# Performance work log

Measured on AMD Instinct MI355X. Metric: run time of the kernel, lower is better.

## Reference

```python
import jax, jax.numpy as jnp
import numpy as np

N = 100000   # nodes
E = 1600000  # edges (before self loops)
F = 64       # num_features
H = 64       # hidden_channels
C = 10       # num_classes
G = 128      # graphs in batch
NEG_SLOPE = 0.2


def setup_inputs() -> dict:
    key = jax.random.key(0)
    ks = jax.random.split(key, 16)
    x = jax.random.normal(ks[0], (N, F), dtype=jnp.float32)
    edge_index = jax.random.randint(ks[1], (2, E), 0, N, dtype=jnp.int64)
    batch = jnp.sort(jax.random.randint(ks[2], (N,), 0, G, dtype=jnp.int64))
    def glorot(k, shape):
        fan = shape[0] + shape[-1]
        return jax.random.uniform(k, shape, jnp.float32, -1.0, 1.0) * np.sqrt(6.0 / fan)
    return {
        "x": x, "edge_index": edge_index, "batch": batch,
        # GATConv 1 (F -> H)
        "W1": glorot(ks[3], (F, H)), "as1": glorot(ks[4], (H,)), "ad1": glorot(ks[5], (H,)), "b1": jnp.zeros((H,), jnp.float32),
        # GATConv 2 (H -> H)
        "W2": glorot(ks[6], (H, H)), "as2": glorot(ks[7], (H,)), "ad2": glorot(ks[8], (H,)), "b2": jnp.zeros((H,), jnp.float32),
        # MLP head
        "mw1": glorot(ks[9], (H, H)), "mb1": jnp.zeros((H,), jnp.float32),
        "mw2": glorot(ks[10], (H, C)), "mb2": jnp.zeros((C,), jnp.float32),
    }


def gat_conv(x, src, dst, W, a_s, a_d, b):
    # x: [N, Fin] -> h: [N, Fout]
    h = x @ W
    # per-node attention halves, gathered per edge (heads=1)
    al_s = h @ a_s   # [N]
    al_d = h @ a_d   # [N]
    e = jax.nn.leaky_relu(al_s[src] + al_d[dst], NEG_SLOPE)  # [E']
    # segment softmax over incoming edges of each destination node
    m = jax.ops.segment_max(e, dst, num_segments=N)
    ex = jnp.exp(e - m[dst])
    denom = jax.ops.segment_sum(ex, dst, num_segments=N)
    alpha = ex / denom[dst]                                   # [E']
    # weighted scatter-add of source features
    out = jax.ops.segment_sum(alpha[:, None] * h[src], dst, num_segments=N)
    return out + b


def reference(x, edge_index, batch, W1, as1, ad1, b1, W2, as2, ad2, b2, mw1, mb1, mw2, mb2):
    # add self loops (PyG GATConv default)
    loop = jnp.arange(N, dtype=edge_index.dtype)
    src = jnp.concatenate([edge_index[0], loop])
    dst = jnp.concatenate([edge_index[1], loop])

    h = gat_conv(x, src, dst, W1, as1, ad1, b1)
    h = jax.nn.elu(h)  # dropout p=0.5 is identity in eval mode
    h = gat_conv(h, src, dst, W2, as2, ad2, b2)
    h = jax.nn.elu(h)

    h = jax.nn.relu(h @ mw1 + mb1) @ mw2 + mb2   # MLP [N, C]
    return jax.ops.segment_sum(h, batch, num_segments=G)  # global_add_pool [G, C]
```

## Files before the change

### kernel.cpp

```cpp
#include <hip/hip_runtime.h>
#include <hip/hip_bf16.h>
#include <math.h>

#define SHIFT 20.0f
#define T_PER 32
#define TILE (256 * T_PER)
#define BCAP 5248
#define LS_T 1024
#define MS_LDS 53248

typedef __bf16 bf16x8 __attribute__((ext_vector_type(8)));
typedef float  f32x4  __attribute__((ext_vector_type(4)));

__device__ __forceinline__ unsigned f2bf(float f) {
    unsigned u = __float_as_uint(f);
    return (u + 0x7fffu + ((u >> 16) & 1u)) >> 16;
}

__global__ void setup_kernel(int* __restrict__ bcur, int K2,
                             float* __restrict__ Pz, int nPz,
                             const float* __restrict__ W1,
                             const float* __restrict__ as1, const float* __restrict__ ad1,
                             const float* __restrict__ W2,
                             const float* __restrict__ as2, const float* __restrict__ ad2,
                             const float* __restrict__ mw1,
                             uint4* __restrict__ Wf1, uint4* __restrict__ Wf2,
                             uint4* __restrict__ mwf)
{
    int t = threadIdx.x;
    if (blockIdx.x == 0) {
        for (int i = t; i < K2; i += 256) bcur[i * 16] = i * BCAP;
        for (int i = t; i < nPz; i += 256) Pz[i] = 0.f;
        return;
    }
    __shared__ float wasad[256];
    {
        int k = t & 63;
        const float* W  = (t < 128) ? W1 : W2;
        const float* av = (t < 64) ? as1 : (t < 128) ? ad1 : (t < 192) ? as2 : ad2;
        float s = 0.f;
        for (int n = 0; n < 64; n++) s = fmaf(W[k * 64 + n], av[n], s);
        wasad[t] = s;
    }
    __syncthreads();

    for (int idx = t; idx < 1792; idx += 256) {
        const float* W; const float* wv; uint4* dst; int rem;
        if (idx < 640)       { rem = idx;        W = W1;  wv = &wasad[0];   dst = Wf1; }
        else if (idx < 1280) { rem = idx - 640;  W = W2;  wv = &wasad[128]; dst = Wf2; }
        else                 { rem = idx - 1280; W = mw1; wv = nullptr;     dst = mwf; }
        int pair = rem >> 6, l = rem & 63;
        int tt = pair >> 1, s = pair & 1;
        int kb = s * 32 + (l >> 4) * 8;
        unsigned d[4];
        if (tt < 4) {
            int n = tt * 16 + (l & 15);
            #pragma unroll
            for (int j = 0; j < 4; j++)
                d[j] = f2bf(W[(kb + 2 * j) * 64 + n]) |
                       (f2bf(W[(kb + 2 * j + 1) * 64 + n]) << 16);
        } else {
            int n0 = l & 15;
            #pragma unroll
            for (int j = 0; j < 4; j++) {
                float v0 = (n0 == 0) ? wv[kb + 2 * j]     : (n0 == 1) ? wv[64 + kb + 2 * j]     : 0.f;
                float v1 = (n0 == 0) ? wv[kb + 2 * j + 1] : (n0 == 1) ? wv[64 + kb + 2 * j + 1] : 0.f;
                d[j] = f2bf(v0) | (f2bf(v1) << 16);
            }
        }
        dst[pair * 64 + l] = make_uint4(d[0], d[1], d[2], d[3]);
    }
}

__device__ __forceinline__ void multisplit_body(
    unsigned char* ldsraw, const int* __restrict__ esrc, const int* __restrict__ edst,
    int* __restrict__ bcur, unsigned* __restrict__ pairbuf,
    int nE, int tot, int K2, int tile)
{
    int* lcur   = (int*)ldsraw;
    int* ldelta = lcur + 512;
    unsigned* seg = (unsigned*)(ldelta + 512);
    unsigned short* bkt = (unsigned short*)(seg + TILE);
    int t = threadIdx.x;
    int base = tile * TILE;
    int cnt_tile = min(TILE, tot - base);

    for (int i = t; i < 512; i += 256) lcur[i] = 0;
    __syncthreads();

    #pragma unroll
    for (int i = 0; i < T_PER; i++) {
        int e = base + t + i * 256;
        if (e < tot) {
            int d = (e < nE) ? edst[e] : (e - nE);
            atomicAdd(&lcur[d >> 8], 1);
        }
    }
    __syncthreads();

    if (t < 64) {
        int c[8]; int s = 0;
        #pragma unroll
        for (int k = 0; k < 8; k++) { c[k] = lcur[t * 8 + k]; s += c[k]; }
        int run = s;
        #pragma unroll
        for (int off = 1; off < 64; off <<= 1) {
            int u = __shfl_up(run, off);
            if (t >= off) run += u;
        }
        int st = run - s;
        #pragma unroll
        for (int k = 0; k < 8; k++) {
            int slot = t * 8 + k;
            lcur[slot] = st;
            if (c[k] > 0 && slot < K2)
                ldelta[slot] = atomicAdd(&bcur[slot * 16], c[k]) - st;
            st += c[k];
        }
    }
    __syncthreads();

    #pragma unroll
    for (int i = 0; i < T_PER; i++) {
        int e = base + t + i * 256;
        if (e < tot) {
            int s = (e < nE) ? esrc[e] : (e - nE);
            int d = (e < nE) ? edst[e] : (e - nE);
            int b = d >> 8;
            int p = atomicAdd(&lcur[b], 1);
            seg[p] = ((unsigned)s << 8) | (unsigned)(d & 255);
            bkt[p] = (unsigned short)b;
        }
    }
    __syncthreads();

    for (int j = t; j < cnt_tile; j += 256)
        pairbuf[j + ldelta[bkt[j]]] = seg[j];
}

__device__ __forceinline__ void gemm_body(
    unsigned char* lds, const void* __restrict__ Xv, int x_is_bf16,
    const uint4* __restrict__ Wf, __hip_bfloat16* __restrict__ Hout,
    float* __restrict__ als, float* __restrict__ ald, int nN, int b0)
{
    int t = threadIdx.x, lane = t & 63, wv = t >> 6;

    uint4 wf[10];
    #pragma unroll
    for (int p = 0; p < 10; p++) wf[p] = Wf[p * 64 + lane];

    if (x_is_bf16) {
        const uint4* X4 = (const uint4*)Xv;
        int limit = nN * 8;
        #pragma unroll
        for (int k = 0; k < 8; k++) {
            int dst = t + k * 256;
            int idx = b0 * 8 + dst;
            if (idx < limit) {
                int r = dst >> 3, c = dst & 7;
                *(uint4*)(lds + r * 144 + c * 16) = X4[idx];
            }
        }
    } else {
        const float4* Xf = (const float4*)Xv;
        int limit = nN * 16;
        #pragma unroll
        for (int k = 0; k < 16; k++) {
            int dst = t + k * 256;
            int idx = b0 * 16 + dst;
            if (idx < limit) {
                float4 v = Xf[idx];
                uint2 r2;
                r2.x = f2bf(v.x) | (f2bf(v.y) << 16);
                r2.y = f2bf(v.z) | (f2bf(v.w) << 16);
                int r = dst >> 4, c = dst & 15;
                *(uint2*)(lds + r * 144 + c * 8) = r2;
            }
        }
    }
    __syncthreads();

    f32x4 acc[4][5] = {};
    int rbase = wv * 64;
    #pragma unroll
    for (int s = 0; s < 2; s++) {
        #pragma unroll
        for (int rf = 0; rf < 4; rf++) {
            const uint4 av = *(const uint4*)(lds + (rbase + rf * 16 + (lane & 15)) * 144
                                                 + s * 64 + (lane >> 4) * 16);
            bf16x8 a = __builtin_bit_cast(bf16x8, av);
            #pragma unroll
            for (int tt = 0; tt < 5; tt++) {
                bf16x8 b = __builtin_bit_cast(bf16x8, wf[tt * 2 + s]);
                acc[rf][tt] = __builtin_amdgcn_mfma_f32_16x16x32_bf16(a, b, acc[rf][tt], 0, 0, 0);
            }
        }
    }

    int q = lane >> 4, c = lane & 15;
    #pragma unroll
    for (int rf = 0; rf < 4; rf++) {
        #pragma unroll
        for (int r = 0; r < 4; r++) {
            int n = b0 + rbase + rf * 16 + q * 4 + r;
            if (n < nN) {
                #pragma unroll
                for (int tt = 0; tt < 4; tt++)
                    Hout[(size_t)n * 64 + tt * 16 + c] = __float2bfloat16(acc[rf][tt][r]);
                if (c == 0)      als[n] = acc[rf][4][r];
                else if (c == 1) ald[n] = acc[rf][4][r];
            }
        }
    }
}

__global__ __launch_bounds__(256) void ms_gemm_kernel(
    const int* __restrict__ esrc, const int* __restrict__ edst,
    int* __restrict__ bcur, unsigned* __restrict__ pairbuf,
    int nE, int nN, int K2, int nTiles,
    const void* __restrict__ Xv, const uint4* __restrict__ Wf,
    __hip_bfloat16* __restrict__ Hout,
    float* __restrict__ als, float* __restrict__ ald)
{
    __shared__ __align__(16) unsigned char lds[MS_LDS];
    if (blockIdx.x < nTiles) {
        multisplit_body(lds, esrc, edst, bcur, pairbuf, nE, nE + nN, K2, blockIdx.x);
    } else {
        gemm_body(lds, Xv, 0, Wf, Hout, als, ald, nN, (blockIdx.x - nTiles) * 256);
    }
}

__global__ __launch_bounds__(256) void gemm_att_mfma(
    const void* __restrict__ Xv, int x_is_bf16,
    const uint4* __restrict__ Wf,
    __hip_bfloat16* __restrict__ Hout,
    float* __restrict__ als, float* __restrict__ ald, int nN)
{
    __shared__ __align__(16) unsigned char lds[256 * 144];
    gemm_body(lds, Xv, x_is_bf16, Wf, Hout, als, ald, nN, blockIdx.x * 256);
}

__global__ __launch_bounds__(LS_T) void local_scatter_kernel(
    const unsigned* __restrict__ pairbuf, const int* __restrict__ bcur,
    int2* __restrict__ rp2, int* __restrict__ csr_src, int nN, int K2)
{
    __shared__ unsigned seg[BCAP];
    __shared__ int lh[256];
    __shared__ int cur[256];
    int b = blockIdx.x;
    int t = threadIdx.x;
    int d0 = b * 256;
    int nd = min(256, nN - d0);
    int lo = b * BCAP;
    int hi = bcur[b * 16];
    int len = min(hi - lo, BCAP);

    if (t < 256) lh[t] = 0;
    for (int j = t; j < len; j += LS_T) seg[j] = pairbuf[lo + j];
    __syncthreads();
    for (int j = t; j < len; j += LS_T) atomicAdd(&lh[seg[j] & 255u], 1);
    __syncthreads();

    if (t < 64) {
        int b4 = t * 4;
        int c0 = lh[b4], c1 = lh[b4 + 1], c2 = lh[b4 + 2], c3 = lh[b4 + 3];
        int tot4 = c0 + c1 + c2 + c3;
        int run = tot4;
        #pragma unroll
        for (int off = 1; off < 64; off <<= 1) {
            int u = __shfl_up(run, off);
            if (t >= off) run += u;
        }
        int e0 = lo + run - tot4;
        int e1 = e0 + c0, e2 = e1 + c1, e3 = e2 + c2;
        cur[b4] = e0; cur[b4 + 1] = e1; cur[b4 + 2] = e2; cur[b4 + 3] = e3;
        if (b4 < nd)     rp2[d0 + b4]     = make_int2(e0, c0);
        if (b4 + 1 < nd) rp2[d0 + b4 + 1] = make_int2(e1, c1);
        if (b4 + 2 < nd) rp2[d0 + b4 + 2] = make_int2(e2, c2);
        if (b4 + 3 < nd) rp2[d0 + b4 + 3] = make_int2(e3, c3);
    }
    __syncthreads();

    for (int j = t; j < len; j += LS_T) {
        unsigned w = seg[j];
        int pos = atomicAdd(&cur[w & 255u], 1);
        csr_src[pos] = (int)(w >> 8);
    }
}

__global__ __launch_bounds__(256) void pull_kernel(
    const int* __restrict__ csr_src, const int2* __restrict__ rp2,
    const unsigned* __restrict__ Hu,
    const float* __restrict__ als, const float* __restrict__ ald,
    const float* __restrict__ bias,
    __hip_bfloat162* __restrict__ out2, int dlo, int dhi)
{
    int lane = threadIdx.x & 63;
    int half = lane >> 5;
    int fl = lane & 31;
    int wid  = (blockIdx.x * blockDim.x + threadIdx.x) >> 6;
    int nw   = (gridDim.x * blockDim.x) >> 6;
    float2 bl2 = ((const float2*)bias)[fl];

    for (int d = dlo + wid; d < dhi; d += nw) {
        int2 rp = rp2[d];
        int s0 = rp.x, m = rp.y;
        float aldd = ald[d];
        float aclo = 0.f, achi = 0.f, den = 0.f;

        for (int base = 0; base < m; base += 64) {
            int j = base + lane;
            bool v = (j < m);
            int sl = v ? csr_src[s0 + j] : 0;
            float ex = 0.f;
            if (v) {
                float sc = als[sl] + aldd;
                sc = (sc > 0.f) ? sc : 0.2f * sc;
                ex = __expf(sc - SHIFT);
            }
            float es = ex;
            #pragma unroll
            for (int off = 32; off > 0; off >>= 1) es += __shfl_xor(es, off);
            den += es;

            int mm = min(64, m - base);
            int sA = __shfl(sl, half), sB = __shfl(sl, 2 + half);
            float eA = __shfl(ex, half), eB = __shfl(ex, 2 + half);
            unsigned dA = Hu[((unsigned)sA << 5) | fl];
            unsigned dB = Hu[((unsigned)sB << 5) | fl];
            for (int i2 = 0; i2 < mm; i2 += 4) {
                int i4 = (i2 + 4) & 63;
                int   sA2 = __shfl(sl, i4 + half);
                int   sB2 = __shfl(sl, i4 + 2 + half);
                float eA2 = __shfl(ex, i4 + half);
                float eB2 = __shfl(ex, i4 + 2 + half);
                unsigned dA2 = Hu[((unsigned)sA2 << 5) | fl];
                unsigned dB2 = Hu[((unsigned)sB2 << 5) | fl];
                aclo = fmaf(eA, __uint_as_float(dA << 16), aclo);
                achi = fmaf(eA, __uint_as_float(dA & 0xffff0000u), achi);
                aclo = fmaf(eB, __uint_as_float(dB << 16), aclo);
                achi = fmaf(eB, __uint_as_float(dB & 0xffff0000u), achi);
                sA = sA2; sB = sB2; eA = eA2; eB = eB2; dA = dA2; dB = dB2;
            }
        }
        aclo += __shfl_xor(aclo, 32);
        achi += __shfl_xor(achi, 32);
        float v0 = aclo / den + bl2.x;
        float v1 = achi / den + bl2.y;
        v0 = (v0 > 0.f) ? v0 : expm1f(v0);
        v1 = (v1 > 0.f) ? v1 : expm1f(v1);
        if (half == 0) {
            __hip_bfloat162 pk;
            pk.x = __float2bfloat16(v0);
            pk.y = __float2bfloat16(v1);
            out2[((unsigned)d << 5) | fl] = pk;
        }
    }
}

__global__ __launch_bounds__(256) void mlp_pool_mfma(
    const uint4* __restrict__ Hin,
    const uint4* __restrict__ mwf, const float* __restrict__ mb1,
    const int* __restrict__ batch,
    float* __restrict__ P, float* __restrict__ Pcnt, int nN)
{
    __shared__ __align__(16) unsigned char lds[256 * 144];
    int t = threadIdx.x, lane = t & 63, wv = t >> 6;
    int b0 = blockIdx.x * 256;

    uint4 wf[8];
    #pragma unroll
    for (int p = 0; p < 8; p++) wf[p] = mwf[p * 64 + lane];

    int limit = nN * 8;
    #pragma unroll
    for (int k = 0; k < 8; k++) {
        int dst = t + k * 256;
        int idx = b0 * 8 + dst;
        if (idx < limit) {
            int r = dst >> 3, c = dst & 7;
            *(uint4*)(lds + r * 144 + c * 16) = Hin[idx];
        }
    }
    __syncthreads();

    f32x4 acc[4][4] = {};
    int rbase = wv * 64;
    #pragma unroll
    for (int s = 0; s < 2; s++) {
        #pragma unroll
        for (int rf = 0; rf < 4; rf++) {
            const uint4 av = *(const uint4*)(lds + (rbase + rf * 16 + (lane & 15)) * 144
                                                 + s * 64 + (lane >> 4) * 16);
            bf16x8 a = __builtin_bit_cast(bf16x8, av);
            #pragma unroll
            for (int tt = 0; tt < 4; tt++) {
                bf16x8 b = __builtin_bit_cast(bf16x8, wf[tt * 2 + s]);
                acc[rf][tt] = __builtin_amdgcn_mfma_f32_16x16x32_bf16(a, b, acc[rf][tt], 0, 0, 0);
            }
        }
    }

    int q = lane >> 4, c = lane & 15;
    float bl0 = mb1[c], bl1 = mb1[16 + c], bl2 = mb1[32 + c], bl3 = mb1[48 + c];
    float r0 = 0.f, r1 = 0.f, r2 = 0.f, r3 = 0.f, ccnt = 0.f;
    int gcur = -1;
    #pragma unroll
    for (int rf = 0; rf < 4; rf++) {
        #pragma unroll
        for (int r = 0; r < 4; r++) {
            int n = b0 + rbase + rf * 16 + q * 4 + r;
            if (n < nN) {
                int g = batch[n];
                if (g != gcur) {
                    if (gcur >= 0) {
                        atomicAdd(&P[(size_t)gcur * 64 + c],      r0);
                        atomicAdd(&P[(size_t)gcur * 64 + 16 + c], r1);
                        atomicAdd(&P[(size_t)gcur * 64 + 32 + c], r2);
                        atomicAdd(&P[(size_t)gcur * 64 + 48 + c], r3);
                        if (c == 0) atomicAdd(&Pcnt[gcur], ccnt);
                    }
                    gcur = g; r0 = r1 = r2 = r3 = 0.f; ccnt = 0.f;
                }
                r0 += fmaxf(acc[rf][0][r] + bl0, 0.f);
                r1 += fmaxf(acc[rf][1][r] + bl1, 0.f);
                r2 += fmaxf(acc[rf][2][r] + bl2, 0.f);
                r3 += fmaxf(acc[rf][3][r] + bl3, 0.f);
                ccnt += 1.f;
            }
        }
    }
    if (gcur >= 0) {
        atomicAdd(&P[(size_t)gcur * 64 + c],      r0);
        atomicAdd(&P[(size_t)gcur * 64 + 16 + c], r1);
        atomicAdd(&P[(size_t)gcur * 64 + 32 + c], r2);
        atomicAdd(&P[(size_t)gcur * 64 + 48 + c], r3);
        if (c == 0) atomicAdd(&Pcnt[gcur], ccnt);
    }
}

__global__ void head_out_kernel(const float* __restrict__ P,
                                const float* __restrict__ Pcnt,
                                const float* __restrict__ mw2,
                                const float* __restrict__ mb2,
                                float* __restrict__ out, int nOut)
{
    int t = blockIdx.x * blockDim.x + threadIdx.x;
    if (t >= nOut) return;
    int g = t / 10, j = t % 10;
    float s = mb2[j] * Pcnt[g];
    const float* pr = P + (size_t)g * 64;
    #pragma unroll
    for (int k = 0; k < 64; k++) s = fmaf(pr[k], mw2[k * 10 + j], s);
    out[t] = s;
}

extern "C" void kernel_launch(void* const* d_in, const int* in_sizes, int n_in,
                              void* d_out, int out_size, void* d_ws, size_t ws_size,
                              hipStream_t stream)
{
    const float* x   = (const float*)d_in[0];
    const int*  eidx = (const int*)d_in[1];
    const int* batch = (const int*)d_in[2];
    const float* W1  = (const float*)d_in[3];
    const float* as1 = (const float*)d_in[4];
    const float* ad1 = (const float*)d_in[5];
    const float* b1  = (const float*)d_in[6];
    const float* W2  = (const float*)d_in[7];
    const float* as2 = (const float*)d_in[8];
    const float* ad2 = (const float*)d_in[9];
    const float* b2  = (const float*)d_in[10];
    const float* mw1 = (const float*)d_in[11];
    const float* mb1 = (const float*)d_in[12];
    const float* mw2 = (const float*)d_in[13];
    const float* mb2 = (const float*)d_in[14];
    float* out = (float*)d_out;

    int nN = in_sizes[0] / 64;
    int nE = in_sizes[1] / 2;
    int tot = nE + nN;
    int K2 = (nN + 255) >> 8;
    int G  = out_size / 10;
    const int* esrc = eidx;
    const int* edst = eidx + nE;

    float* ws = (float*)d_ws;
    size_t NF = (size_t)nN * 64;
    size_t capTot = (size_t)K2 * BCAP;
    float* bufA   = ws;
    float* bufB   = ws + NF;
    float* als    = ws + 2 * NF;
    float* ald    = als + nN;
    int2* rp2     = (int2*)(ald + nN);
    int* csr_src  = (int*)(rp2 + nN);
    int* bcur     = csr_src + capTot;
    float* P      = (float*)(bcur + K2 * 16 + 15);
    float* Pcnt   = P + (size_t)G * 64;
    uintptr_t wb  = ((uintptr_t)(Pcnt + G) + 255) & ~(uintptr_t)255;
    uint4* Wf1    = (uint4*)wb;
    uint4* Wf2    = Wf1 + 640;
    uint4* mwf    = Wf2 + 640;
    unsigned* pairbuf = (unsigned*)bufA;
    __hip_bfloat16* hbf = (__hip_bfloat16*)bufB;

    dim3 blk(256);
    int nTiles = (tot + TILE - 1) / TILE;
    int nT256 = (nN + 255) / 256;
    int nHalf = nN / 2;

    setup_kernel<<<2, blk, 0, stream>>>(bcur, K2, P, G * 64 + G,
                                        W1, as1, ad1, W2, as2, ad2, mw1,
                                        Wf1, Wf2, mwf);
    ms_gemm_kernel<<<nTiles + nT256, blk, 0, stream>>>(
        esrc, edst, bcur, pairbuf, nE, nN, K2, nTiles,
        x, Wf1, hbf, als, ald);
    local_scatter_kernel<<<K2, dim3(LS_T), 0, stream>>>(pairbuf, bcur, rp2,
                                                        csr_src, nN, K2);

    pull_kernel<<<2048, blk, 0, stream>>>(csr_src, rp2, (const unsigned*)hbf,
                                          als, ald, b1,
                                          (__hip_bfloat162*)bufA, 0, nHalf);
    pull_kernel<<<2048, blk, 0, stream>>>(csr_src, rp2, (const unsigned*)hbf,
                                          als, ald, b1,
                                          (__hip_bfloat162*)bufA, nHalf, nN);
    gemm_att_mfma<<<nT256, blk, 0, stream>>>(bufA, 1, Wf2, hbf, als, ald, nN);
    pull_kernel<<<2048, blk, 0, stream>>>(csr_src, rp2, (const unsigned*)hbf,
                                          als, ald, b2,
                                          (__hip_bfloat162*)bufA, 0, nHalf);
    pull_kernel<<<2048, blk, 0, stream>>>(csr_src, rp2, (const unsigned*)hbf,
                                          als, ald, b2,
                                          (__hip_bfloat162*)bufA, nHalf, nN);

    mlp_pool_mfma<<<nT256, blk, 0, stream>>>((const uint4*)bufA, mwf, mb1,
                                             batch, P, Pcnt, nN);
    head_out_kernel<<<(out_size + 255) / 256, blk, 0, stream>>>(P, Pcnt, mw2,
                                                                mb2, out, out_size);
}
```

Before: 300.2 us.

## Replace global atomic bucket cursors with per-tile offset table and tile-local writes

Multisplit tiles no longer take a global atomicAdd on per-bucket cursors to scatter pairs into bucket regions. Each tile now writes its locally sorted pairs contiguously at its own offset and records per-bucket start offsets in a small per-tile table. The local scatter kernel prefix-sums those offsets across tiles and gathers each bucket's pieces from every tile. This removes global atomics, the bucket-id LDS array and the cursor init, which lowers LDS use. In exchange each bucket gathers many small pieces (about 210 tiles) with less coalesced reads.

After: 296.0 us. No clear change (-1.4%).

```diff
diff --git a/kernel.cpp b/kernel.cpp
--- a/kernel.cpp
+++ b/kernel.cpp
@@ -7,7 +7,7 @@
 #define TILE (256 * T_PER)
 #define BCAP 5248
 #define LS_T 1024
-#define MS_LDS 53248
+#define MS_LDS 36864
 
 typedef __bf16 bf16x8 __attribute__((ext_vector_type(8)));
 typedef float  f32x4  __attribute__((ext_vector_type(4)));
@@ -17,8 +17,7 @@
     return (u + 0x7fffu + ((u >> 16) & 1u)) >> 16;
 }
 
-__global__ void setup_kernel(int* __restrict__ bcur, int K2,
-                             float* __restrict__ Pz, int nPz,
+__global__ void setup_kernel(float* __restrict__ Pz, int nPz,
                              const float* __restrict__ W1,
                              const float* __restrict__ as1, const float* __restrict__ ad1,
                              const float* __restrict__ W2,
@@ -29,7 +28,6 @@
 {
     int t = threadIdx.x;
     if (blockIdx.x == 0) {
-        for (int i = t; i < K2; i += 256) bcur[i * 16] = i * BCAP;
         for (int i = t; i < nPz; i += 256) Pz[i] = 0.f;
         return;
     }
@@ -74,13 +72,11 @@
 
 __device__ __forceinline__ void multisplit_body(
     unsigned char* ldsraw, const int* __restrict__ esrc, const int* __restrict__ edst,
-    int* __restrict__ bcur, unsigned* __restrict__ pairbuf,
-    int nE, int tot, int K2, int tile)
+    unsigned short* __restrict__ stab, unsigned* __restrict__ pairbuf,
+    int nE, int tot, int K2, int TW, int tile)
 {
     int* lcur   = (int*)ldsraw;
-    int* ldelta = lcur + 512;
-    unsigned* seg = (unsigned*)(ldelta + 512);
-    unsigned short* bkt = (unsigned short*)(seg + TILE);
+    unsigned* seg = (unsigned*)(lcur + 512);
     int t = threadIdx.x;
     int base = tile * TILE;
     int cnt_tile = min(TILE, tot - base);
@@ -113,8 +109,7 @@
         for (int k = 0; k < 8; k++) {
             int slot = t * 8 + k;
             lcur[slot] = st;
-            if (c[k] > 0 && slot < K2)
-                ldelta[slot] = atomicAdd(&bcur[slot * 16], c[k]) - st;
+            if (slot <= K2) stab[(size_t)tile * TW + slot] = (unsigned short)st;
             st += c[k];
         }
     }
@@ -126,16 +121,14 @@
         if (e < tot) {
             int s = (e < nE) ? esrc[e] : (e - nE);
             int d = (e < nE) ? edst[e] : (e - nE);
-            int b = d >> 8;
-            int p = atomicAdd(&lcur[b], 1);
+            int p = atomicAdd(&lcur[d >> 8], 1);
             seg[p] = ((unsigned)s << 8) | (unsigned)(d & 255);
-            bkt[p] = (unsigned short)b;
         }
     }
     __syncthreads();
 
     for (int j = t; j < cnt_tile; j += 256)
-        pairbuf[j + ldelta[bkt[j]]] = seg[j];
+        pairbuf[base + j] = seg[j];
 }
 
 __device__ __forceinline__ void gemm_body(
@@ -216,15 +209,15 @@
 
 __global__ __launch_bounds__(256) void ms_gemm_kernel(
     const int* __restrict__ esrc, const int* __restrict__ edst,
-    int* __restrict__ bcur, unsigned* __restrict__ pairbuf,
-    int nE, int nN, int K2, int nTiles,
+    unsigned short* __restrict__ stab, unsigned* __restrict__ pairbuf,
+    int nE, int nN, int K2, int TW, int nTiles,
     const void* __restrict__ Xv, const uint4* __restrict__ Wf,
     __hip_bfloat16* __restrict__ Hout,
     float* __restrict__ als, float* __restrict__ ald)
 {
     __shared__ __align__(16) unsigned char lds[MS_LDS];
     if (blockIdx.x < nTiles) {
-        multisplit_body(lds, esrc, edst, bcur, pairbuf, nE, nE + nN, K2, blockIdx.x);
+        multisplit_body(lds, esrc, edst, stab, pairbuf, nE, nE + nN, K2, TW, blockIdx.x);
     } else {
         gemm_body(lds, Xv, 0, Wf, Hout, als, ald, nN, (blockIdx.x - nTiles) * 256);
     }
@@ -241,22 +234,60 @@
 }
 
 __global__ __launch_bounds__(LS_T) void local_scatter_kernel(
-    const unsigned* __restrict__ pairbuf, const int* __restrict__ bcur,
-    int2* __restrict__ rp2, int* __restrict__ csr_src, int nN, int K2)
+    const unsigned* __restrict__ pairbuf, const unsigned short* __restrict__ stab,
+    int2* __restrict__ rp2, int* __restrict__ csr_src,
+    int nN, int K2, int TW, int nTiles)
 {
     __shared__ unsigned seg[BCAP];
     __shared__ int lh[256];
     __shared__ int cur[256];
+    __shared__ int tstart[256], toff[256], tlen[256];
+    __shared__ int ltot;
     int b = blockIdx.x;
     int t = threadIdx.x;
+    int wv = t >> 6, lane = t & 63;
     int d0 = b * 256;
     int nd = min(256, nN - d0);
     int lo = b * BCAP;
-    int hi = bcur[b * 16];
-    int len = min(hi - lo, BCAP);
 
     if (t < 256) lh[t] = 0;
-    for (int j = t; j < len; j += LS_T) seg[j] = pairbuf[lo + j];
+    if (t < 64) {
+        int ln[4], gs[4]; int s = 0;
+        #pragma unroll
+        for (int k = 0; k < 4; k++) {
+            int tile = t * 4 + k;
+            int l = 0, g = 0;
+            if (tile < nTiles) {
+                int st = stab[(size_t)tile * TW + b];
+                int en = stab[(size_t)tile * TW + b + 1];
+                l = en - st;
+                g = tile * TILE + st;
+            }
+            ln[k] = l; gs[k] = g; s += l;
+        }
+        int run = s;
+        #pragma unroll
+        for (int off = 1; off < 64; off <<= 1) {
+            int u = __shfl_up(run, off);
+            if (t >= off) run += u;
+        }
+        int off0 = run - s;
+        #pragma unroll
+        for (int k = 0; k < 4; k++) {
+            int tile = t * 4 + k;
+            if (tile < nTiles) { toff[tile] = off0; tstart[tile] = gs[k]; tlen[tile] = ln[k]; }
+            off0 += ln[k];
+        }
+        if (t == 63) ltot = run;
+    }
+    __syncthreads();
+    int len = min(ltot, BCAP);
+
+    for (int tile = wv; tile < nTiles; tile += LS_T / 64) {
+        int l = tlen[tile], o = toff[tile], g = tstart[tile];
+        for (int j = lane; j < l; j += 64)
+            if (o + j < BCAP) seg[o + j] = pairbuf[g + j];
+    }
     __syncthreads();
     for (int j = t; j < len; j += LS_T) atomicAdd(&lh[seg[j] & 255u], 1);
     __syncthreads();
@@ -480,21 +511,28 @@
     int nE = in_sizes[1] / 2;
     int tot = nE + nN;
     int K2 = (nN + 255) >> 8;
+    int TW = K2 + 1;
     int G  = out_size / 10;
     const int* esrc = eidx;
     const int* edst = eidx + nE;
 
+    int nTiles = (tot + TILE - 1) / TILE;
+    int nT256 = (nN + 255) / 256;
+    int nHalf = nN / 2;
+
     float* ws = (float*)d_ws;
     size_t NF = (size_t)nN * 64;
     size_t capTot = (size_t)K2 * BCAP;
+    size_t pbTot  = (size_t)nTiles * TILE;
     float* bufA   = ws;
     float* bufB   = ws + NF;
     float* als    = ws + 2 * NF;
     float* ald    = als + nN;
     int2* rp2     = (int2*)(ald + nN);
     int* csr_src  = (int*)(rp2 + nN);
-    int* bcur     = csr_src + capTot;
-    float* P      = (float*)(bcur + K2 * 16 + 15);
+    unsigned short* stab = (unsigned short*)(csr_src + capTot);
+    float* P      = (float*)(((uintptr_t)(stab + (size_t)nTiles * TW) + 63)
+                             & ~(uintptr_t)63);
     float* Pcnt   = P + (size_t)G * 64;
     uintptr_t wb  = ((uintptr_t)(Pcnt + G) + 255) & ~(uintptr_t)255;
     uint4* Wf1    = (uint4*)wb;
@@ -502,20 +540,19 @@
     uint4* mwf    = Wf2 + 640;
     unsigned* pairbuf = (unsigned*)bufA;
     __hip_bfloat16* hbf = (__hip_bfloat16*)bufB;
+    (void)pbTot;
 
     dim3 blk(256);
-    int nTiles = (tot + TILE - 1) / TILE;
-    int nT256 = (nN + 255) / 256;
-    int nHalf = nN / 2;
-
-    setup_kernel<<<2, blk, 0, stream>>>(bcur, K2, P, G * 64 + G,
+
+    setup_kernel<<<2, blk, 0, stream>>>(P, G * 64 + G,
                                         W1, as1, ad1, W2, as2, ad2, mw1,
                                         Wf1, Wf2, mwf);
     ms_gemm_kernel<<<nTiles + nT256, blk, 0, stream>>>(
-        esrc, edst, bcur, pairbuf, nE, nN, K2, nTiles,
+        esrc, edst, stab, pairbuf, nE, nN, K2, TW, nTiles,
         x, Wf1, hbf, als, ald);
-    local_scatter_kernel<<<K2, dim3(LS_T), 0, stream>>>(pairbuf, bcur, rp2,
-                                                        csr_src, nN, K2);
+    local_scatter_kernel<<<K2, dim3(LS_T), 0, stream>>>(pairbuf, stab, rp2,
+                                                        csr_src, nN, K2, TW,
+                                                        nTiles);
 
     pull_kernel<<<2048, blk, 0, stream>>>(csr_src, rp2, (const unsigned*)hbf,
                                           als, ald, b1,
```
